# Kernel optimization log

Hardware: AMD Instinct MI355X
Metric: run time of the kernel (lower is better)

Reference implementation:

```python
import jax, jax.numpy as jnp
import numpy as np

N, E, G = 50000, 800000, 64
IN, EDGE = 128, 16
HID, H = 32, 4
FHID, HF = 64, 4
OUT = 16
NEG_SLOPE = 0.2


def _segment_softmax(logits, seg, num):
    m = jax.ops.segment_max(logits, seg, num_segments=num)
    m = jnp.where(jnp.isfinite(m), m, 0.0)
    p = jnp.exp(logits - m[seg])
    s = jax.ops.segment_sum(p, seg, num_segments=num)
    return p / (s[seg] + 1e-16)


def gatv2(x, src, dst, eattr, Wl, bl, Wr, br, We, att, bias, concat):
    # PyG GATv2Conv with add_self_loops=True (edge_attr fill_value='mean')
    n = x.shape[0]
    heads, ch = att.shape
    ones = jnp.ones((src.shape[0],), x.dtype)
    cnt = jax.ops.segment_sum(ones, dst, num_segments=n)
    mean_attr = jax.ops.segment_sum(eattr, dst, num_segments=n) / jnp.maximum(cnt, 1.0)[:, None]
    loop = jnp.arange(n)
    s = jnp.concatenate([src, loop])
    d = jnp.concatenate([dst, loop])
    ea = jnp.concatenate([eattr, mean_attr], axis=0)
    xl = (x @ Wl + bl).reshape(n, heads, ch)   # lin_l (source)
    xr = (x @ Wr + br).reshape(n, heads, ch)   # lin_r (target)
    ee = (ea @ We).reshape(-1, heads, ch)      # lin_edge (no bias)
    z = jax.nn.leaky_relu(xl[s] + xr[d] + ee, NEG_SLOPE)  # [E+N, H, C]
    logits = jnp.einsum('ehc,hc->eh', z, att)
    alpha = _segment_softmax(logits, d, n)
    out = jax.ops.segment_sum(alpha[:, :, None] * xl[s], d, num_segments=n)  # [N, H, C]
    out = out.reshape(n, heads * ch) if concat else out.mean(axis=1)
    return out + bias


def _forward(x, edge_attr, src, dst, batch,
             Wl0, bl0, Wr0, br0, We0, att0, bo0,
             Wlh, blh, Wrh, brh, Weh, atth, boh,
             Wlf, blf, Wrf, brf, Wef, attf, bof,
             Wlin, blin):
    h1 = jax.nn.relu(gatv2(x, src, dst, edge_attr, Wl0, bl0, Wr0, br0, We0, att0, bo0, True))
    h2 = jax.nn.relu(gatv2(h1, src, dst, edge_attr, Wlh, blh, Wrh, brh, Weh, atth, boh, True))
    h3 = jax.nn.relu(gatv2(h2, src, dst, edge_attr, Wlf, blf, Wrf, brf, Wef, attf, bof, False))
    # global_mean_pool over graphs
    gsum = jax.ops.segment_sum(h3, batch, num_segments=G)
    gcnt = jax.ops.segment_sum(jnp.ones((h3.shape[0],), h3.dtype), batch, num_segments=G)
    g = gsum / jnp.maximum(gcnt, 1.0)[:, None]
    return g @ Wlin + blin  # final_dropout inactive in eval mode


def setup_inputs():
    key = jax.random.key(0)
    ks = jax.random.split(key, 20)
    def p(i, shape, fan_in):
        return jax.random.normal(ks[i], shape, jnp.float32) / np.sqrt(fan_in)
    z = lambda *s: jnp.zeros(s, jnp.float32)
    return {
        'x': jax.random.normal(ks[0], (N, IN), jnp.float32),
        'edge_index': jax.random.randint(ks[1], (2, E), 0, N),
        'batch': jnp.sort(jax.random.randint(ks[2], (N,), 0, G)),
        'edge_attr': jax.random.normal(ks[3], (E, EDGE), jnp.float32),
        'Wl0': p(4, (IN, H * HID), IN), 'bl0': z(H * HID),
        'Wr0': p(5, (IN, H * HID), IN), 'br0': z(H * HID),
        'We0': p(6, (EDGE, H * HID), EDGE), 'att0': p(7, (H, HID), HID), 'bo0': z(H * HID),
        'Wlh': p(8, (H * HID, H * HID), H * HID), 'blh': z(H * HID),
        'Wrh': p(9, (H * HID, H * HID), H * HID), 'brh': z(H * HID),
        'Weh': p(10, (EDGE, H * HID), EDGE), 'atth': p(11, (H, HID), HID), 'boh': z(H * HID),
        'Wlf': p(12, (H * HID, HF * FHID), H * HID), 'blf': z(HF * FHID),
        'Wrf': p(13, (H * HID, HF * FHID), H * HID), 'brf': z(HF * FHID),
        'Wef': p(14, (EDGE, HF * FHID), EDGE), 'attf': p(15, (HF, FHID), FHID), 'bof': z(FHID),
        'Wlin': p(16, (FHID, OUT), FHID), 'blin': z(OUT),
    }


def reference(x, edge_index, batch, edge_attr, Wl0, bl0, Wr0, br0, We0, att0, bo0, Wlh, blh, Wrh, brh, Weh, atth, boh, Wlf, blf, Wrf, brf, Wef, attf, bof, Wlin, blin):
    return _forward(x, edge_attr, edge_index[0], edge_index[1], batch,
                    Wl0, bl0, Wr0, br0, We0, att0, bo0,
                    Wlh, blh, Wrh, brh, Weh, atth, boh,
                    Wlf, blf, Wrf, brf, Wef, attf, bof,
                    Wlin, blin)
```

## Files before the change

### kernel.cpp

```cpp
#include <hip/hip_runtime.h>
#include <cstddef>

#define NSLOPE 0.2f

constexpr int NN = 50000;
constexpr int EE = 800000;
constexpr int GG = 64;
constexpr int SCAN_B = 1024;

typedef unsigned short ushort_t;
typedef unsigned int uint_t;
typedef __bf16 bhalf;
typedef bhalf bhalf8 __attribute__((ext_vector_type(8)));
typedef float floatx4 __attribute__((ext_vector_type(4)));
typedef _Float16 half_t;
typedef half_t half2_t __attribute__((ext_vector_type(2)));

__device__ __forceinline__ ushort_t f2b(float f) {
  unsigned int u = __float_as_uint(f);
  unsigned int r = (u + 0x7fffu + ((u >> 16) & 1u)) >> 16;
  return (ushort_t)r;
}
__device__ __forceinline__ float b2f(ushort_t b) {
  return __uint_as_float(((unsigned int)b) << 16);
}
__device__ __forceinline__ uint_t packh2(float a, float b) {
  half2_t h = {(half_t)a, (half_t)b};
  return __builtin_bit_cast(uint_t, h);
}
__device__ __forceinline__ float dot2acc(uint_t ea, half2_t w, float c) {
  half2_t a = __builtin_bit_cast(half2_t, ea);
#if __has_builtin(__builtin_amdgcn_fdot2)
  return __builtin_amdgcn_fdot2(a, w, c, false);
#else
  return c + (float)a.x * (float)w.x + (float)a.y * (float)w.y;
#endif
}

__global__ void hist_kernel(const int* __restrict__ dst, int* __restrict__ hist, int E) {
  int e = blockIdx.x * blockDim.x + threadIdx.x;
  if (e < E) atomicAdd(&hist[dst[e]], 1);
}

__global__ void scan_block_kernel(const int* __restrict__ in, int* __restrict__ out,
                                  int* __restrict__ bsum, int n) {
  __shared__ int tmp[SCAN_B];
  int gid = blockIdx.x * SCAN_B + threadIdx.x;
  int v = (gid < n) ? in[gid] : 0;
  tmp[threadIdx.x] = v;
  __syncthreads();
  for (int off = 1; off < SCAN_B; off <<= 1) {
    int t = (threadIdx.x >= off) ? tmp[threadIdx.x - off] : 0;
    __syncthreads();
    tmp[threadIdx.x] += t;
    __syncthreads();
  }
  if (gid < n) out[gid] = tmp[threadIdx.x];
  if (threadIdx.x == SCAN_B - 1) bsum[blockIdx.x] = tmp[threadIdx.x];
}

__global__ void scan_totals_kernel(const int* __restrict__ bsum, int* __restrict__ boff, int nb) {
  if (blockIdx.x == 0 && threadIdx.x == 0) {
    int run = 0;
    for (int i = 0; i < nb; ++i) { boff[i] = run; run += bsum[i]; }
  }
}

__global__ void add_offsets_kernel(int* __restrict__ rowptr, const int* __restrict__ boff,
                                   int* __restrict__ cursor, int n) {
  int gid = blockIdx.x * SCAN_B + threadIdx.x;
  if (gid == 0) { rowptr[0] = 0; cursor[0] = 0; }
  if (gid < n) {
    int v = rowptr[1 + gid] + boff[blockIdx.x];
    rowptr[1 + gid] = v;
    if (1 + gid < n) cursor[1 + gid] = v;
  }
}

__global__ void scatter_perm_kernel(const int* __restrict__ dst, int* __restrict__ cursor,
                                    int* __restrict__ perm, int E) {
  int e = blockIdx.x * blockDim.x + threadIdx.x;
  if (e < E) {
    int pos = atomicAdd(&cursor[dst[e]], 1);
    perm[pos] = e;
  }
}

__global__ void permute_kernel(const int* __restrict__ perm, const int* __restrict__ src,
                               const float* __restrict__ eattr,
                               int* __restrict__ srcp, uint_t* __restrict__ eah, int E) {
  int j = blockIdx.x * blockDim.x + threadIdx.x;
  if (j >= E) return;
  int e = perm[j];
  srcp[j] = src[e];
  const float* a = eattr + (size_t)e * 16;
  uint_t o[8];
#pragma unroll
  for (int k2 = 0; k2 < 8; ++k2) o[k2] = packh2(a[2 * k2], a[2 * k2 + 1]);
  uint4* b = reinterpret_cast<uint4*>(eah + (size_t)j * 8);
  b[0] = make_uint4(o[0], o[1], o[2], o[3]);
  b[1] = make_uint4(o[4], o[5], o[6], o[7]);
}

__global__ void mean_attr_kernel(const int* __restrict__ rowptr, const uint_t* __restrict__ eah,
                                 uint_t* __restrict__ meanattr_h, int N) {
  int idx = blockIdx.x * blockDim.x + threadIdx.x;
  if (idx >= N * 8) return;
  int i = idx >> 3, k2 = idx & 7;
  int beg = rowptr[i], end = rowptr[i + 1];
  float ax = 0.f, ay = 0.f;
  for (int j = beg; j < end; ++j) {
    half2_t h = __builtin_bit_cast(half2_t, eah[(size_t)j * 8 + k2]);
    ax += (float)h.x; ay += (float)h.y;
  }
  int c = end - beg; if (c < 1) c = 1;
  float inv = 1.f / (float)c;
  meanattr_h[idx] = packh2(ax * inv, ay * inv);
}

__global__ void f2b_kernel(const float* __restrict__ in, ushort_t* __restrict__ out, int n4) {
  int i = blockIdx.x * blockDim.x + threadIdx.x;
  if (i >= n4) return;
  float4 v = reinterpret_cast<const float4*>(in)[i];
  ushort4 o = make_ushort4(f2b(v.x), f2b(v.y), f2b(v.z), f2b(v.w));
  reinterpret_cast<ushort4*>(out)[i] = o;
}

__global__ void prep_w_kernel(const float* W0, ushort_t* T0, int n0,
                              const float* W1, ushort_t* T1, int n1,
                              const float* W2, ushort_t* T2, int n2,
                              const float* W3, ushort_t* T3, int n3,
                              const float* W4, ushort_t* T4, int n4,
                              const float* W5, ushort_t* T5, int n5) {
  const float* W; ushort_t* T; int Nc;
  switch (blockIdx.y) {
    case 0: W = W0; T = T0; Nc = n0; break;
    case 1: W = W1; T = T1; Nc = n1; break;
    case 2: W = W2; T = T2; Nc = n2; break;
    case 3: W = W3; T = T3; Nc = n3; break;
    case 4: W = W4; T = T4; Nc = n4; break;
    default: W = W5; T = T5; Nc = n5; break;
  }
  int idx = blockIdx.x * blockDim.x + threadIdx.x;
  if (idx >= Nc * 128) return;
  int n = idx >> 7, k = idx & 127;
  T[idx] = f2b(W[(size_t)k * Nc + n]);
}

__global__ __launch_bounds__(256) void gemm_bt_dual_bf16(
    const ushort_t* __restrict__ Xb,
    const ushort_t* __restrict__ Wt0, const float* __restrict__ b0, ushort_t* __restrict__ Y0,
    const ushort_t* __restrict__ Wt1, const float* __restrict__ b1, ushort_t* __restrict__ Y1,
    int M, int Nc) {
  constexpr int K = 128, BM = 128, LDT = 136;
  __shared__ ushort_t Als[BM * LDT];
  __shared__ ushort_t Bls[BM * LDT];
  int nb = Nc >> 7;
  int half = blockIdx.y / nb;
  int cb = blockIdx.y % nb;
  const ushort_t* Wt = half ? Wt1 : Wt0;
  const float* bias = half ? b1 : b0;
  ushort_t* Y = half ? Y1 : Y0;
  int r0 = blockIdx.x * BM;
  int col0 = cb * 128;
  int tid = threadIdx.x;
  {
    int rl = tid >> 5;
    int kq = (tid & 31) * 4;
#pragma unroll
    for (int s = 0; s < 16; ++s) {
      int row = rl + s * 8;
      int grow = r0 + row;
      ushort4 v = make_ushort4(0, 0, 0, 0);
      if (grow < M) v = *reinterpret_cast<const ushort4*>(Xb + (size_t)grow * K + kq);
      *reinterpret_cast<ushort4*>(&Als[row * LDT + kq]) = v;
      ushort4 wv = *reinterpret_cast<const ushort4*>(Wt + (size_t)(col0 + row) * K + kq);
      *reinterpret_cast<ushort4*>(&Bls[row * LDT + kq]) = wv;
    }
  }
  __syncthreads();
  int lane = tid & 63;
  int w = tid >> 6;
  int m0 = (w >> 1) * 64;
  int n0 = (w & 1) * 64;
  int rin = lane & 15, quad = lane >> 4;
  floatx4 acc[4][4];
#pragma unroll
  for (int i = 0; i < 4; ++i)
#pragma unroll
    for (int j = 0; j < 4; ++j) acc[i][j] = (floatx4){0.f, 0.f, 0.f, 0.f};
#pragma unroll
  for (int kt = 0; kt < 4; ++kt) {
    int ko = kt * 32 + quad * 8;
    bhalf8 af[4], bf[4];
#pragma unroll
    for (int i = 0; i < 4; ++i)
      af[i] = *reinterpret_cast<const bhalf8*>(&Als[(m0 + i * 16 + rin) * LDT + ko]);
#pragma unroll
    for (int i = 0; i < 4; ++i)
      bf[i] = *reinterpret_cast<const bhalf8*>(&Bls[(n0 + i * 16 + rin) * LDT + ko]);
#pragma unroll
    for (int mi = 0; mi < 4; ++mi)
#pragma unroll
      for (int ni = 0; ni < 4; ++ni)
        acc[mi][ni] = __builtin_amdgcn_mfma_f32_16x16x32_bf16(af[mi], bf[ni], acc[mi][ni], 0, 0, 0);
  }
#pragma unroll
  for (int ni = 0; ni < 4; ++ni) {
    int gcol = col0 + n0 + ni * 16 + rin;
    float bb = bias[gcol];
#pragma unroll
    for (int mi = 0; mi < 4; ++mi) {
      int growb = r0 + m0 + mi * 16 + quad * 4;
#pragma unroll
      for (int r = 0; r < 4; ++r) {
        int grow = growb + r;
        if (grow < M) Y[(size_t)grow * Nc + gcol] = f2b(acc[mi][ni][r] + bb);
      }
    }
  }
}

template <int VPL>
__device__ __forceinline__ void loadb(const ushort_t* p, float* v) {
  if constexpr (VPL == 2) {
    ushort2 t = *reinterpret_cast<const ushort2*>(p);
    v[0] = b2f(t.x); v[1] = b2f(t.y);
  } else {
    ushort4 t = *reinterpret_cast<const ushort4*>(p);
    v[0] = b2f(t.x); v[1] = b2f(t.y); v[2] = b2f(t.z); v[3] = b2f(t.w);
  }
}
template <int VPL>
__device__ __forceinline__ void storeb(ushort_t* p, const float* v) {
  if constexpr (VPL == 2) {
    *reinterpret_cast<ushort2*>(p) = make_ushort2(f2b(v[0]), f2b(v[1]));
  } else {
    *reinterpret_cast<ushort4*>(p) = make_ushort4(f2b(v[0]), f2b(v[1]), f2b(v[2]), f2b(v[3]));
  }
}

template <int VPL>
__device__ __forceinline__ float lrelu_dot(const float* xv, const float* rv,
                                           const half2_t (*wepk)[VPL], const float* areg,
                                           const uint_t* ea) {
  float part = 0.f;
#pragma unroll
  for (int j = 0; j < VPL; ++j) {
    float z = xv[j] + rv[j];
#pragma unroll
    for (int k2 = 0; k2 < 8; ++k2) z = dot2acc(ea[k2], wepk[k2][j], z);
    float zl = fmaxf(z, NSLOPE * z);
    part = fmaf(zl, areg[j], part);
  }
  part += __shfl_xor(part, 1);
  part += __shfl_xor(part, 2);
  part += __shfl_xor(part, 4);
  part += __shfl_xor(part, 8);
  return part;
}

template <int EB, int VPL, int C>
__device__ __forceinline__ void process_group(
    const int* __restrict__ srcp, const uint_t* __restrict__ eah, int j,
    const ushort_t* __restrict__ xl, int lane, const float* rv,
    const half2_t (*wepk)[VPL], const float* areg,
    float& s, float* acc) {
  int sn[EB];
#pragma unroll
  for (int u = 0; u < EB; ++u) sn[u] = srcp[j + u];
  float xv[EB][VPL];
#pragma unroll
  for (int u = 0; u < EB; ++u) loadb<VPL>(xl + (size_t)sn[u] * C + lane * VPL, xv[u]);
  float lg[EB];
#pragma unroll
  for (int u = 0; u < EB; ++u) {
    const uint_t* ap = eah + (size_t)(j + u) * 8;
    uint_t ea[8];
#pragma unroll
    for (int k2 = 0; k2 < 8; ++k2) ea[k2] = ap[k2];
    lg[u] = lrelu_dot<VPL>(xv[u], rv, wepk, areg, ea);
  }
  float p[EB], ps = 0.f;
#pragma unroll
  for (int u = 0; u < EB; ++u) { p[u] = __expf(lg[u]); ps += p[u]; }
  s += ps;
#pragma unroll
  for (int jj = 0; jj < VPL; ++jj) {
    float t = p[0] * xv[0][jj];
#pragma unroll
    for (int u = 1; u < EB; ++u) t = fmaf(p[u], xv[u][jj], t);
    acc[jj] += t;
  }
}

template <int VPL, int C>
__device__ __forceinline__ void process_edge(
    int sn, const uint_t* ea,
    const ushort_t* __restrict__ xl, int lane, const float* rv,
    const half2_t (*wepk)[VPL], const float* areg,
    float& s, float* acc) {
  float xv[VPL];
  loadb<VPL>(xl + (size_t)sn * C + lane * VPL, xv);
  float lg = lrelu_dot<VPL>(xv, rv, wepk, areg, ea);
  float p = __expf(lg);
  s += p;
#pragma unroll
  for (int jj = 0; jj < VPL; ++jj) acc[jj] = fmaf(p, xv[jj], acc[jj]);
}

template <int C, bool FINAL>
__global__ __launch_bounds__(256) void gat_fused_kernel(
    const int* __restrict__ rowptr,
    const int* __restrict__ srcp, const uint_t* __restrict__ eah,
    const uint_t* __restrict__ meanattr_h,
    const ushort_t* __restrict__ xl, const ushort_t* __restrict__ xr,
    const float* __restrict__ We,
    const float* __restrict__ att,
    const float* __restrict__ bias, ushort_t* __restrict__ hout, int N) {
  constexpr int VPL = C / 64;
  const int lane = threadIdx.x & 63;
  int d = __builtin_amdgcn_readfirstlane(blockIdx.x * (blockDim.x >> 6) + (threadIdx.x >> 6));
  if (d >= N) return;

  half2_t wepk[8][VPL];
  float areg[VPL];
#pragma unroll
  for (int k2 = 0; k2 < 8; ++k2)
#pragma unroll
    for (int j = 0; j < VPL; ++j) {
      int ch = lane * VPL + j;
      wepk[k2][j] = (half2_t){(half_t)We[(2 * k2) * C + ch], (half_t)We[(2 * k2 + 1) * C + ch]};
    }
#pragma unroll
  for (int j = 0; j < VPL; ++j) areg[j] = att[lane * VPL + j];

  int beg = rowptr[d], end = rowptr[d + 1];
  float rv[VPL];
  loadb<VPL>(xr + (size_t)d * C + lane * VPL, rv);

  float s = 0.f;
  float acc[VPL];
#pragma unroll
  for (int j = 0; j < VPL; ++j) acc[j] = 0.f;

  int j = beg;
  if constexpr (C == 128) {
    for (; j + 8 <= end; j += 8)
      process_group<8, VPL, C>(srcp, eah, j, xl, lane, rv, wepk, areg, s, acc);
  }
  for (; j + 4 <= end; j += 4)
    process_group<4, VPL, C>(srcp, eah, j, xl, lane, rv, wepk, areg, s, acc);
  for (; j + 2 <= end; j += 2)
    process_group<2, VPL, C>(srcp, eah, j, xl, lane, rv, wepk, areg, s, acc);
  for (; j < end; ++j)
    process_group<1, VPL, C>(srcp, eah, j, xl, lane, rv, wepk, areg, s, acc);
  {
    const uint_t* mp = meanattr_h + (size_t)d * 8;
    uint_t ea[8];
#pragma unroll
    for (int k2 = 0; k2 < 8; ++k2) ea[k2] = mp[k2];
    process_edge<VPL, C>(d, ea, xl, lane, rv, wepk, areg, s, acc);
  }

  float inv = 1.f / (s + 1e-16f);
  if constexpr (!FINAL) {
    float res[VPL];
#pragma unroll
    for (int jj = 0; jj < VPL; ++jj) {
      float v = acc[jj] * inv + bias[lane * VPL + jj];
      res[jj] = v > 0.f ? v : 0.f;
    }
    storeb<VPL>(hout + (size_t)d * C + lane * VPL, res);
  } else {
    float v[VPL];
#pragma unroll
    for (int jj = 0; jj < VPL; ++jj) v[jj] = acc[jj] * inv;
#pragma unroll
    for (int jj = 0; jj < VPL; ++jj) {
      v[jj] += __shfl_xor(v[jj], 16);
      v[jj] += __shfl_xor(v[jj], 32);
    }
    if (lane < 16) {
      float res[VPL];
#pragma unroll
      for (int jj = 0; jj < VPL; ++jj) {
        float val = 0.25f * v[jj] + bias[lane * VPL + jj];
        res[jj] = val > 0.f ? val : 0.f;
      }
      storeb<VPL>(hout + (size_t)d * 64 + lane * VPL, res);
    }
  }
}

__global__ __launch_bounds__(256) void pool_kernel(
    const ushort_t* __restrict__ h3, const int* __restrict__ batch,
    float* __restrict__ gsum, float* __restrict__ gcnt, int N) {
  const int lane = threadIdx.x & 63;
  const int w = blockIdx.x * (blockDim.x >> 6) + (threadIdx.x >> 6);
  const int nw = gridDim.x * (blockDim.x >> 6);
  const int chunk = (N + nw - 1) / nw;
  int i0 = w * chunk;
  int i1 = i0 + chunk; if (i1 > N) i1 = N;
  if (i0 >= i1) return;
  int cur = batch[i0];
  float acc = 0.f;
  int cnt = 0;
  for (int i = i0; i < i1; ++i) {
    int g = batch[i];
    if (g != cur) {
      atomicAdd(&gsum[(size_t)cur * 64 + lane], acc);
      if (lane == 0) atomicAdd(&gcnt[cur], (float)cnt);
      acc = 0.f; cnt = 0; cur = g;
    }
    acc += b2f(h3[(size_t)i * 64 + lane]);
    ++cnt;
  }
  atomicAdd(&gsum[(size_t)cur * 64 + lane], acc);
  if (lane == 0) atomicAdd(&gcnt[cur], (float)cnt);
}

__global__ void final_kernel(const float* __restrict__ gsum, const float* __restrict__ gcnt,
                             const float* __restrict__ Wlin, const float* __restrict__ blin,
                             float* __restrict__ out) {
  int idx = blockIdx.x * blockDim.x + threadIdx.x;
  if (idx >= GG * 16) return;
  int g = idx >> 4, o = idx & 15;
  float c = gcnt[g];
  c = c > 1.f ? c : 1.f;
  float inv = 1.f / c;
  float acc = blin[o];
  for (int f = 0; f < 64; ++f) acc = fmaf(gsum[(size_t)g * 64 + f] * inv, Wlin[f * 16 + o], acc);
  out[idx] = acc;
}

extern "C" void kernel_launch(void* const* d_in, const int* in_sizes, int n_in,
                              void* d_out, int out_size, void* d_ws, size_t ws_size,
                              hipStream_t stream) {
  (void)in_sizes; (void)n_in; (void)out_size; (void)ws_size;
  const float* x     = (const float*)d_in[0];
  const int*   eidx  = (const int*)d_in[1];
  const int*   batch = (const int*)d_in[2];
  const float* eattr = (const float*)d_in[3];
  const float* Wl0 = (const float*)d_in[4];  const float* bl0 = (const float*)d_in[5];
  const float* Wr0 = (const float*)d_in[6];  const float* br0 = (const float*)d_in[7];
  const float* We0 = (const float*)d_in[8];  const float* att0 = (const float*)d_in[9];
  const float* bo0 = (const float*)d_in[10];
  const float* Wlh = (const float*)d_in[11]; const float* blh = (const float*)d_in[12];
  const float* Wrh = (const float*)d_in[13]; const float* brh = (const float*)d_in[14];
  const float* Weh = (const float*)d_in[15]; const float* atth = (const float*)d_in[16];
  const float* boh = (const float*)d_in[17];
  const float* Wlf = (const float*)d_in[18]; const float* blf = (const float*)d_in[19];
  const float* Wrf = (const float*)d_in[20]; const float* brf = (const float*)d_in[21];
  const float* Wef = (const float*)d_in[22]; const float* attf = (const float*)d_in[23];
  const float* bof = (const float*)d_in[24];
  const float* Wlin = (const float*)d_in[25]; const float* blin = (const float*)d_in[26];

  const int* src = eidx;
  const int* dst = eidx + EE;

  char* ws = (char*)d_ws;
  size_t off = 0;
  auto take = [&](size_t bytes) -> void* {
    void* p = ws + off;
    off += (bytes + 1023) & ~(size_t)1023;
    return p;
  };
  ushort_t* xl     = (ushort_t*)take((size_t)NN * 256 * 2);
  ushort_t* xr     = (ushort_t*)take((size_t)NN * 256 * 2);
  ushort_t* hb     = (ushort_t*)take((size_t)NN * 128 * 2);
  ushort_t* xb     = (ushort_t*)take((size_t)NN * 128 * 2);
  uint_t* meanattr_h = (uint_t*)take((size_t)NN * 8 * 4);
  int* hist        = (int*)take((size_t)NN * 4);
  int* rowptr      = (int*)take((size_t)(NN + 1) * 4);
  int* cursor      = (int*)take((size_t)NN * 4);
  int* perm        = (int*)take((size_t)EE * 4);
  int* bsum        = (int*)take(256);
  int* boff        = (int*)take(256);
  float* gsum      = (float*)take((size_t)GG * 64 * 4);
  float* gcnt      = (float*)take((size_t)GG * 4);
  ushort_t* wtl0   = (ushort_t*)take((size_t)128 * 128 * 2);
  ushort_t* wtr0   = (ushort_t*)take((size_t)128 * 128 * 2);
  ushort_t* wtlh   = (ushort_t*)take((size_t)128 * 128 * 2);
  ushort_t* wtrh   = (ushort_t*)take((size_t)128 * 128 * 2);
  ushort_t* wtlf   = (ushort_t*)take((size_t)256 * 128 * 2);
  ushort_t* wtrf   = (ushort_t*)take((size_t)256 * 128 * 2);
  int* srcp        = (int*)take((size_t)EE * 4);
  uint_t* eah      = (uint_t*)take((size_t)EE * 8 * 4);

  hipMemsetAsync(hist, 0, (size_t)NN * 4, stream);
  hipMemsetAsync(gsum, 0, (size_t)GG * 64 * 4, stream);
  hipMemsetAsync(gcnt, 0, (size_t)GG * 4, stream);
  hist_kernel<<<(EE + 255) / 256, 256, 0, stream>>>(dst, hist, EE);
  int nsb = (NN + SCAN_B - 1) / SCAN_B;
  scan_block_kernel<<<nsb, SCAN_B, 0, stream>>>(hist, rowptr + 1, bsum, NN);
  scan_totals_kernel<<<1, 64, 0, stream>>>(bsum, boff, nsb);
  add_offsets_kernel<<<nsb, SCAN_B, 0, stream>>>(rowptr, boff, cursor, NN);
  scatter_perm_kernel<<<(EE + 255) / 256, 256, 0, stream>>>(dst, cursor, perm, EE);
  permute_kernel<<<(EE + 255) / 256, 256, 0, stream>>>(perm, src, eattr, srcp, eah, EE);
  mean_attr_kernel<<<(NN * 8 + 255) / 256, 256, 0, stream>>>(rowptr, eah, meanattr_h, NN);
  prep_w_kernel<<<dim3(128, 6), 256, 0, stream>>>(Wl0, wtl0, 128, Wr0, wtr0, 128,
                                                  Wlh, wtlh, 128, Wrh, wtrh, 128,
                                                  Wlf, wtlf, 256, Wrf, wtrf, 256);
  f2b_kernel<<<(NN * 128 / 4 + 255) / 256, 256, 0, stream>>>(x, xb, NN * 128 / 4);

  const int AGG_BLOCKS = (NN + 3) / 4;
  const int GEMM_MB = (NN + 127) / 128;

  gemm_bt_dual_bf16<<<dim3(GEMM_MB, 2), 256, 0, stream>>>(xb, wtl0, bl0, xl, wtr0, br0, xr, NN, 128);
  gat_fused_kernel<128, false><<<AGG_BLOCKS, 256, 0, stream>>>(
      rowptr, srcp, eah, meanattr_h, xl, xr, We0, att0, bo0, hb, NN);
  gemm_bt_dual_bf16<<<dim3(GEMM_MB, 2), 256, 0, stream>>>(hb, wtlh, blh, xl, wtrh, brh, xr, NN, 128);
  gat_fused_kernel<128, false><<<AGG_BLOCKS, 256, 0, stream>>>(
      rowptr, srcp, eah, meanattr_h, xl, xr, Weh, atth, boh, hb, NN);
  gemm_bt_dual_bf16<<<dim3(GEMM_MB, 4), 256, 0, stream>>>(hb, wtlf, blf, xl, wtrf, brf, xr, NN, 256);
  gat_fused_kernel<256, true><<<AGG_BLOCKS, 256, 0, stream>>>(
      rowptr, srcp, eah, meanattr_h, xl, xr, Wef, attf, bof, hb, NN);
  pool_kernel<<<128, 256, 0, stream>>>(hb, batch, gsum, gcnt, NN);
  final_kernel<<<4, 256, 0, stream>>>(gsum, gcnt, Wlin, blin, (float*)d_out);
}
```

Measured before the change: 715.7 us.

## Fuse edge scatter/permute, prefetch next edge group, prepack edge weights and exp2

Merges the scatter and permute kernels so edge attributes and sources are written straight to their CSR position, dropping the perm array and one pass over the edges. Mean-attr now uses one wavefront per node with shuffle reduction instead of one thread per node and component. The aggregation kernel software-pipelines gathers, loading the next group of source features while computing the current one. Edge weights are prepacked to half2 once and att is pre-scaled by log2(e) so exp2f can be used. The prefetch raises register pressure and may reduce occupancy.

```diff
diff --git a/kernel.cpp b/kernel.cpp
--- a/kernel.cpp
+++ b/kernel.cpp
@@ -77,45 +77,45 @@
   }
 }
 
-__global__ void scatter_perm_kernel(const int* __restrict__ dst, int* __restrict__ cursor,
-                                    int* __restrict__ perm, int E) {
+__global__ void scatter_fused_kernel(const int* __restrict__ dst, const int* __restrict__ src,
+                                     const float* __restrict__ eattr, int* __restrict__ cursor,
+                                     int* __restrict__ srcp, uint_t* __restrict__ eah, int E) {
   int e = blockIdx.x * blockDim.x + threadIdx.x;
-  if (e < E) {
-    int pos = atomicAdd(&cursor[dst[e]], 1);
-    perm[pos] = e;
-  }
-}
-
-__global__ void permute_kernel(const int* __restrict__ perm, const int* __restrict__ src,
-                               const float* __restrict__ eattr,
-                               int* __restrict__ srcp, uint_t* __restrict__ eah, int E) {
-  int j = blockIdx.x * blockDim.x + threadIdx.x;
-  if (j >= E) return;
-  int e = perm[j];
-  srcp[j] = src[e];
-  const float* a = eattr + (size_t)e * 16;
-  uint_t o[8];
-#pragma unroll
-  for (int k2 = 0; k2 < 8; ++k2) o[k2] = packh2(a[2 * k2], a[2 * k2 + 1]);
-  uint4* b = reinterpret_cast<uint4*>(eah + (size_t)j * 8);
-  b[0] = make_uint4(o[0], o[1], o[2], o[3]);
-  b[1] = make_uint4(o[4], o[5], o[6], o[7]);
-}
-
-__global__ void mean_attr_kernel(const int* __restrict__ rowptr, const uint_t* __restrict__ eah,
-                                 uint_t* __restrict__ meanattr_h, int N) {
-  int idx = blockIdx.x * blockDim.x + threadIdx.x;
-  if (idx >= N * 8) return;
-  int i = idx >> 3, k2 = idx & 7;
-  int beg = rowptr[i], end = rowptr[i + 1];
+  if (e >= E) return;
+  const float4* a = reinterpret_cast<const float4*>(eattr + (size_t)e * 16);
+  float4 f0 = a[0], f1 = a[1], f2 = a[2], f3 = a[3];
+  int pos = atomicAdd(&cursor[dst[e]], 1);
+  srcp[pos] = src[e];
+  uint4 o0 = make_uint4(packh2(f0.x, f0.y), packh2(f0.z, f0.w),
+                        packh2(f1.x, f1.y), packh2(f1.z, f1.w));
+  uint4 o1 = make_uint4(packh2(f2.x, f2.y), packh2(f2.z, f2.w),
+                        packh2(f3.x, f3.y), packh2(f3.z, f3.w));
+  uint4* b = reinterpret_cast<uint4*>(eah + (size_t)pos * 8);
+  b[0] = o0; b[1] = o1;
+}
+
+__global__ __launch_bounds__(256) void mean_attr_kernel(
+    const int* __restrict__ rowptr, const uint_t* __restrict__ eah,
+    uint_t* __restrict__ meanattr_h, int N) {
+  const int lane = threadIdx.x & 63;
+  int d = blockIdx.x * (blockDim.x >> 6) + (threadIdx.x >> 6);
+  if (d >= N) return;
+  int beg = rowptr[d], end = rowptr[d + 1];
+  int k2 = lane & 7;
+  int sub = lane >> 3;
   float ax = 0.f, ay = 0.f;
-  for (int j = beg; j < end; ++j) {
+  for (int j = beg + sub; j < end; j += 8) {
     half2_t h = __builtin_bit_cast(half2_t, eah[(size_t)j * 8 + k2]);
     ax += (float)h.x; ay += (float)h.y;
   }
-  int c = end - beg; if (c < 1) c = 1;
-  float inv = 1.f / (float)c;
-  meanattr_h[idx] = packh2(ax * inv, ay * inv);
+  ax += __shfl_xor(ax, 8);  ay += __shfl_xor(ay, 8);
+  ax += __shfl_xor(ax, 16); ay += __shfl_xor(ay, 16);
+  ax += __shfl_xor(ax, 32); ay += __shfl_xor(ay, 32);
+  if (sub == 0) {
+    int c = end - beg; if (c < 1) c = 1;
+    float inv = 1.f / (float)c;
+    meanattr_h[(size_t)d * 8 + k2] = packh2(ax * inv, ay * inv);
+  }
 }
 
 __global__ void f2b_kernel(const float* __restrict__ in, ushort_t* __restrict__ out, int n4) {
@@ -145,6 +145,27 @@
   if (idx >= Nc * 128) return;
   int n = idx >> 7, k = idx & 127;
   T[idx] = f2b(W[(size_t)k * Nc + n]);
+}
+
+__global__ void prep_we_kernel(const float* We0, const float* att0, uint_t* w0, float* a0,
+                               const float* We1, const float* att1, uint_t* w1, float* a1,
+                               const float* We2, const float* att2, uint_t* w2, float* a2) {
+  const float* We; const float* att; uint_t* wp; float* ap; int C;
+  switch (blockIdx.y) {
+    case 0: We = We0; att = att0; wp = w0; ap = a0; C = 128; break;
+    case 1: We = We1; att = att1; wp = w1; ap = a1; C = 128; break;
+    default: We = We2; att = att2; wp = w2; ap = a2; C = 256; break;
+  }
+  int idx = blockIdx.x * blockDim.x + threadIdx.x;
+  if (idx >= 9 * C) return;
+  if (idx < 8 * C) {
+    int sh = (C == 256) ? 8 : 7;
+    int k2 = idx >> sh, ch = idx & (C - 1);
+    wp[idx] = packh2(We[(size_t)(2 * k2) * C + ch], We[(size_t)(2 * k2 + 1) * C + ch]);
+  } else {
+    int ch = idx - 8 * C;
+    ap[ch] = att[ch] * 1.44269504f;
+  }
 }
 
 __global__ __launch_bounds__(256) void gemm_bt_dual_bf16(
@@ -241,6 +262,15 @@
 }
 
 template <int VPL>
+__device__ __forceinline__ void unpack_raw(const uint_t* raw, float* xv) {
+#pragma unroll
+  for (int r = 0; r < VPL / 2; ++r) {
+    xv[2 * r]     = __uint_as_float(raw[r] << 16);
+    xv[2 * r + 1] = __uint_as_float(raw[r] & 0xffff0000u);
+  }
+}
+
+template <int VPL>
 __device__ __forceinline__ float lrelu_dot(const float* xv, const float* rv,
                                            const half2_t (*wepk)[VPL], const float* areg,
                                            const uint_t* ea) {
@@ -258,6 +288,52 @@
   part += __shfl_xor(part, 4);
   part += __shfl_xor(part, 8);
   return part;
+}
+
+template <int EB, int VPL>
+__device__ __forceinline__ void load_grp(const int* __restrict__ srcp,
+                                         const ushort_t* __restrict__ xl, int lane, int j,
+                                         uint_t (*xraw)[VPL / 2]) {
+  constexpr int RW = VPL / 2;
+  int sn[EB];
+#pragma unroll
+  for (int u = 0; u < EB; ++u) sn[u] = srcp[j + u];
+#pragma unroll
+  for (int u = 0; u < EB; ++u) {
+    const uint_t* p = reinterpret_cast<const uint_t*>(xl + (size_t)sn[u] * (VPL * 64)) + lane * RW;
+#pragma unroll
+    for (int r = 0; r < RW; ++r) xraw[u][r] = p[r];
+  }
+}
+
+template <int EB, int VPL>
+__device__ __forceinline__ void compute_grp(const uint_t* __restrict__ eah, int j,
+                                            const uint_t (*xraw)[VPL / 2], int lane,
+                                            const float* rv, const half2_t (*wepk)[VPL],
+                                            const float* areg, float& s, float* acc) {
+  float xv[EB][VPL];
+#pragma unroll
+  for (int u = 0; u < EB; ++u) unpack_raw<VPL>(xraw[u], xv[u]);
+  float lg[EB];
+#pragma unroll
+  for (int u = 0; u < EB; ++u) {
+    const uint_t* ap = eah + (size_t)(j + u) * 8;
+    uint_t ea[8];
+#pragma unroll
+    for (int k2 = 0; k2 < 8; ++k2) ea[k2] = ap[k2];
+    lg[u] = lrelu_dot<VPL>(xv[u], rv, wepk, areg, ea);
+  }
+  float p[EB], ps = 0.f;
+#pragma unroll
+  for (int u = 0; u < EB; ++u) { p[u] = exp2f(lg[u]); ps += p[u]; }
+  s += ps;
+#pragma unroll
+  for (int jj = 0; jj < VPL; ++jj) {
+    float t = p[0] * xv[0][jj];
+#pragma unroll
+    for (int u = 1; u < EB; ++u) t = fmaf(p[u], xv[u][jj], t);
+    acc[jj] += t;
+  }
 }
 
 template <int EB, int VPL, int C>
@@ -283,7 +359,7 @@
   }
   float p[EB], ps = 0.f;
 #pragma unroll
-  for (int u = 0; u < EB; ++u) { p[u] = __expf(lg[u]); ps += p[u]; }
+  for (int u = 0; u < EB; ++u) { p[u] = exp2f(lg[u]); ps += p[u]; }
   s += ps;
 #pragma unroll
   for (int jj = 0; jj < VPL; ++jj) {
@@ -303,7 +379,7 @@
   float xv[VPL];
   loadb<VPL>(xl + (size_t)sn * C + lane * VPL, xv);
   float lg = lrelu_dot<VPL>(xv, rv, wepk, areg, ea);
-  float p = __expf(lg);
+  float p = exp2f(lg);
   s += p;
 #pragma unroll
   for (int jj = 0; jj < VPL; ++jj) acc[jj] = fmaf(p, xv[jj], acc[jj]);
@@ -315,46 +391,65 @@
     const int* __restrict__ srcp, const uint_t* __restrict__ eah,
     const uint_t* __restrict__ meanattr_h,
     const ushort_t* __restrict__ xl, const ushort_t* __restrict__ xr,
-    const float* __restrict__ We,
-    const float* __restrict__ att,
+    const uint_t* __restrict__ wep,
+    const float* __restrict__ atts,
     const float* __restrict__ bias, ushort_t* __restrict__ hout, int N) {
   constexpr int VPL = C / 64;
+  constexpr int RW = VPL / 2;
+  constexpr int GEB = (C == 128) ? 8 : 4;
   const int lane = threadIdx.x & 63;
   int d = __builtin_amdgcn_readfirstlane(blockIdx.x * (blockDim.x >> 6) + (threadIdx.x >> 6));
   if (d >= N) return;
 
+  int beg = rowptr[d], end = rowptr[d + 1];
+  int ng = (end - beg) / GEB;
+  int j = beg;
+
+  uint_t xrC[GEB][RW];
+  if (ng > 0) load_grp<GEB, VPL>(srcp, xl, lane, j, xrC);
+
   half2_t wepk[8][VPL];
   float areg[VPL];
 #pragma unroll
   for (int k2 = 0; k2 < 8; ++k2)
 #pragma unroll
-    for (int j = 0; j < VPL; ++j) {
-      int ch = lane * VPL + j;
-      wepk[k2][j] = (half2_t){(half_t)We[(2 * k2) * C + ch], (half_t)We[(2 * k2 + 1) * C + ch]};
-    }
-#pragma unroll
-  for (int j = 0; j < VPL; ++j) areg[j] = att[lane * VPL + j];
-
-  int beg = rowptr[d], end = rowptr[d + 1];
+    for (int jj = 0; jj < VPL; ++jj)
+      wepk[k2][jj] = __builtin_bit_cast(half2_t, wep[k2 * C + lane * VPL + jj]);
+#pragma unroll
+  for (int jj = 0; jj < VPL; ++jj) areg[jj] = atts[lane * VPL + jj];
+
   float rv[VPL];
   loadb<VPL>(xr + (size_t)d * C + lane * VPL, rv);
 
   float s = 0.f;
   float acc[VPL];
 #pragma unroll
-  for (int j = 0; j < VPL; ++j) acc[j] = 0.f;
-
-  int j = beg;
+  for (int jj = 0; jj < VPL; ++jj) acc[jj] = 0.f;
+
+  for (int g = 1; g < ng; ++g) {
+    uint_t xrN[GEB][RW];
+    load_grp<GEB, VPL>(srcp, xl, lane, j + GEB, xrN);
+    compute_grp<GEB, VPL>(eah, j, xrC, lane, rv, wepk, areg, s, acc);
+    j += GEB;
+#pragma unroll
+    for (int u = 0; u < GEB; ++u)
+#pragma unroll
+      for (int r = 0; r < RW; ++r) xrC[u][r] = xrN[u][r];
+  }
+  if (ng > 0) {
+    compute_grp<GEB, VPL>(eah, j, xrC, lane, rv, wepk, areg, s, acc);
+    j += GEB;
+  }
+
   if constexpr (C == 128) {
-    for (; j + 8 <= end; j += 8)
-      process_group<8, VPL, C>(srcp, eah, j, xl, lane, rv, wepk, areg, s, acc);
-  }
-  for (; j + 4 <= end; j += 4)
-    process_group<4, VPL, C>(srcp, eah, j, xl, lane, rv, wepk, areg, s, acc);
+    for (; j + 4 <= end; j += 4)
+      process_group<4, VPL, C>(srcp, eah, j, xl, lane, rv, wepk, areg, s, acc);
+  }
   for (; j + 2 <= end; j += 2)
     process_group<2, VPL, C>(srcp, eah, j, xl, lane, rv, wepk, areg, s, acc);
   for (; j < end; ++j)
     process_group<1, VPL, C>(srcp, eah, j, xl, lane, rv, wepk, areg, s, acc);
+
   {
     const uint_t* mp = meanattr_h + (size_t)d * 8;
     uint_t ea[8];
@@ -474,7 +569,6 @@
   int* hist        = (int*)take((size_t)NN * 4);
   int* rowptr      = (int*)take((size_t)(NN + 1) * 4);
   int* cursor      = (int*)take((size_t)NN * 4);
-  int* perm        = (int*)take((size_t)EE * 4);
   int* bsum        = (int*)take(256);
   int* boff        = (int*)take(256);
   float* gsum      = (float*)take((size_t)GG * 64 * 4);
@@ -487,6 +581,12 @@
   ushort_t* wtrf   = (ushort_t*)take((size_t)256 * 128 * 2);
   int* srcp        = (int*)take((size_t)EE * 4);
   uint_t* eah      = (uint_t*)take((size_t)EE * 8 * 4);
+  uint_t* we0p     = (uint_t*)take((size_t)8 * 128 * 4);
+  uint_t* wehp     = (uint_t*)take((size_t)8 * 128 * 4);
+  uint_t* wefp     = (uint_t*)take((size_t)8 * 256 * 4);
+  float* att0s     = (float*)take((size_t)128 * 4);
+  float* atths     = (float*)take((size_t)128 * 4);
+  float* attfs     = (float*)take((size_t)256 * 4);
 
   hipMemsetAsync(hist, 0, (size_t)NN * 4, stream);
   hipMemsetAsync(gsum, 0, (size_t)GG * 64 * 4, stream);
@@ -496,12 +596,14 @@
   scan_block_kernel<<<nsb, SCAN_B, 0, stream>>>(hist, rowptr + 1, bsum, NN);
   scan_totals_kernel<<<1, 64, 0, stream>>>(bsum, boff, nsb);
   add_offsets_kernel<<<nsb, SCAN_B, 0, stream>>>(rowptr, boff, cursor, NN);
-  scatter_perm_kernel<<<(EE + 255) / 256, 256, 0, stream>>>(dst, cursor, perm, EE);
-  permute_kernel<<<(EE + 255) / 256, 256, 0, stream>>>(perm, src, eattr, srcp, eah, EE);
-  mean_attr_kernel<<<(NN * 8 + 255) / 256, 256, 0, stream>>>(rowptr, eah, meanattr_h, NN);
+  scatter_fused_kernel<<<(EE + 255) / 256, 256, 0, stream>>>(dst, src, eattr, cursor, srcp, eah, EE);
+  mean_attr_kernel<<<(NN + 3) / 4, 256, 0, stream>>>(rowptr, eah, meanattr_h, NN);
   prep_w_kernel<<<dim3(128, 6), 256, 0, stream>>>(Wl0, wtl0, 128, Wr0, wtr0, 128,
                                                   Wlh, wtlh, 128, Wrh, wtrh, 128,
                                                   Wlf, wtlf, 256, Wrf, wtrf, 256);
+  prep_we_kernel<<<dim3(9, 3), 256, 0, stream>>>(We0, att0, we0p, att0s,
+                                                 Weh, atth, wehp, atths,
+                                                 Wef, attf, wefp, attfs);
   f2b_kernel<<<(NN * 128 / 4 + 255) / 256, 256, 0, stream>>>(x, xb, NN * 128 / 4);
 
   const int AGG_BLOCKS = (NN + 3) / 4;
@@ -509,13 +611,13 @@
 
   gemm_bt_dual_bf16<<<dim3(GEMM_MB, 2), 256, 0, stream>>>(xb, wtl0, bl0, xl, wtr0, br0, xr, NN, 128);
   gat_fused_kernel<128, false><<<AGG_BLOCKS, 256, 0, stream>>>(
-      rowptr, srcp, eah, meanattr_h, xl, xr, We0, att0, bo0, hb, NN);
+      rowptr, srcp, eah, meanattr_h, xl, xr, we0p, att0s, bo0, hb, NN);
   gemm_bt_dual_bf16<<<dim3(GEMM_MB, 2), 256, 0, stream>>>(hb, wtlh, blh, xl, wtrh, brh, xr, NN, 128);
   gat_fused_kernel<128, false><<<AGG_BLOCKS, 256, 0, stream>>>(
-      rowptr, srcp, eah, meanattr_h, xl, xr, Weh, atth, boh, hb, NN);
+      rowptr, srcp, eah, meanattr_h, xl, xr, wehp, atths, boh, hb, NN);
   gemm_bt_dual_bf16<<<dim3(GEMM_MB, 4), 256, 0, stream>>>(hb, wtlf, blf, xl, wtrf, brf, xr, NN, 256);
   gat_fused_kernel<256, true><<<AGG_BLOCKS, 256, 0, stream>>>(
-      rowptr, srcp, eah, meanattr_h, xl, xr, Wef, attf, bof, hb, NN);
+      rowptr, srcp, eah, meanattr_h, xl, xr, wefp, attfs, bof, hb, NN);
   pool_kernel<<<128, 256, 0, stream>>>(hb, batch, gsum, gcnt, NN);
   final_kernel<<<4, 256, 0, stream>>>(gsum, gcnt, Wlin, blin, (float*)d_out);
 }
```

New measurement: 730.9 us. 2.1% more time.
